# Performance work log

Hardware: AMD Instinct MI355X
Metric: run time of the kernel (lower is better)

Reference implementation:

```python
import jax, jax.numpy as jnp
import numpy as np

B, S, D, H = 8, 1024, 512, 8
DK = D // H
NEG = -1e30  # stands in for -inf; masked probs are zero-filled afterwards, so math matches


def setup_inputs() -> dict:
    rng = jax.random.key(0)
    ks = jax.random.split(rng, 12)
    f = lambda k, shape: jax.random.normal(k, shape, dtype=jnp.float32)
    w = lambda k: f(k, (D, D)) * 0.02  # stored as (in, out); y = x @ W + b
    return {
        "query": f(ks[0], (B, S, D)),
        "key": f(ks[1], (B, S, D)),
        "value": f(ks[2], (B, S, D)),
        "mask": jax.random.randint(ks[3], (B, 1, S), 0, 2, dtype=jnp.int32),
        "Wq": w(ks[4]), "bq": jnp.zeros((D,), jnp.float32),
        "Wk": w(ks[5]), "bk": jnp.zeros((D,), jnp.float32),
        "Wv": w(ks[6]), "bv": jnp.zeros((D,), jnp.float32),
        "Wo": w(ks[7]), "bo": jnp.zeros((D,), jnp.float32),
    }


def reference(query, key, value, mask, Wq, bq, Wk, bk, Wv, bv, Wo, bo):
    # QKV projections -> (B, H, S, DK)
    def proj(x, W, b):
        return (x @ W + b).reshape(B, -1, H, DK).transpose(0, 2, 1, 3)

    q = proj(query, Wq, bq)
    k = proj(key, Wk, bk)
    v = proj(value, Wv, bv)

    scores = jnp.einsum("bhqd,bhkd->bhqk", q, k) / jnp.sqrt(jnp.float32(DK))
    m = (mask[:, None, :, :] == 0)  # (B, 1, 1, S): True where masked out
    scores = jnp.where(m, NEG, scores)
    attn = jax.nn.softmax(scores, axis=-1)
    attn = jnp.where(m, 0.0, attn)  # dropout rate is 0.0 -> identity

    x = jnp.einsum("bhqk,bhkd->bhqd", attn, v)
    x = x.transpose(0, 2, 1, 3).reshape(B, -1, D)  # (B, S, D)
    return x @ Wo + bo
```

## Files before the change

kernel.cpp:

```cpp
#include <hip/hip_runtime.h>
#include <hip/hip_bf16.h>

#define NB 8
#define NS 1024
#define ND 512
#define NH 8
#define NDK 64

typedef __attribute__((ext_vector_type(8))) short bf16x8;
typedef __attribute__((ext_vector_type(4))) float f32x4;
typedef __attribute__((ext_vector_type(16))) float f32x16;

#define QSCALE 0.18033688011112042f
#define NEGBIG -3.0e38f

#define CVTPK(dst, a, b) \
    asm("v_cvt_pk_bf16_f32 %0, %1, %2" : "=v"(dst) : "v"(a), "v"(b))
#define PLSWAP(a, b) \
    asm("v_permlane32_swap_b32 %0, %1" : "+v"(a), "+v"(b))
#define GLOAD16(gp, lp)                                                        \
    __builtin_amdgcn_global_load_lds(                                          \
        (const __attribute__((address_space(1))) unsigned*)(gp),               \
        (__attribute__((address_space(3))) unsigned*)(lp), 16, 0, 0)
#define VMCNT0() asm volatile("s_waitcnt vmcnt(0)" ::: "memory")
#define SBAR() __builtin_amdgcn_s_barrier()
#define SCHED0() __builtin_amdgcn_sched_barrier(0)

__device__ __forceinline__ unsigned short bfround(float f) {
    union { float f; unsigned u; } v; v.f = f;
    unsigned u = v.u;
    u += 0x7fffu + ((u >> 16) & 1u);
    return (unsigned short)(u >> 16);
}

__device__ __forceinline__ size_t qf_off(int s, int dk) {
    return ((size_t)(((s >> 5) * 4 + (dk >> 4)) * 64 + ((dk >> 3) & 1) * 32 + (s & 31)) << 3) + (dk & 7);
}
__device__ __forceinline__ size_t kf_off(int s, int dk) {
    return ((size_t)(((s >> 6) * 8 + ((s >> 5) & 1) * 4 + (dk >> 4)) * 64 + ((dk >> 3) & 1) * 32 + (s & 31)) << 3) + (dk & 7);
}
__device__ __forceinline__ size_t vf_off(int s, int dk) {
    return ((size_t)(((s >> 6) * 8 + (dk >> 5) * 4 + ((s >> 4) & 3)) * 64 + ((s >> 3) & 1) * 32 + (dk & 31)) << 3) + (s & 7);
}

__global__ __launch_bounds__(256) void wt_kernel(const float* __restrict__ W0,
                                                 const float* __restrict__ W1,
                                                 const float* __restrict__ W2,
                                                 const float* __restrict__ W3,
                                                 unsigned short* __restrict__ wt) {
    __shared__ float sh[64][65];
    const int z = blockIdx.z;
    const float* W = z == 0 ? W0 : z == 1 ? W1 : z == 2 ? W2 : W3;
    unsigned short* out = wt + (size_t)z * ND * ND;
    const int o0 = blockIdx.x * 64, i0 = blockIdx.y * 64;
    const int tx = threadIdx.x & 63;
    const int ty = threadIdx.x >> 6;
    #pragma unroll
    for (int rr = 0; rr < 16; ++rr) {
        const int row = ty * 16 + rr;
        sh[row][tx] = W[(size_t)(i0 + row) * ND + o0 + tx];
    }
    __syncthreads();
    #pragma unroll
    for (int rr = 0; rr < 16; ++rr) {
        const int row = ty * 16 + rr;
        out[(size_t)(o0 + row) * ND + i0 + tx] = bfround(sh[tx][row]);
    }
}

__global__ __launch_bounds__(256) void gemm_qkv(
    const float* __restrict__ A0, const float* __restrict__ A1, const float* __restrict__ A2,
    const unsigned short* __restrict__ wt,
    const float* __restrict__ b0, const float* __restrict__ b1, const float* __restrict__ b2,
    unsigned short* __restrict__ outb) {
    __shared__ float Asf[2][128 * 32];
    __shared__ unsigned short Bs[2][128 * 32];
    const int t = threadIdx.x;
    const int lane = t & 63, w = t >> 6;
    const int wr = w >> 1, wc = w & 1;
    const int lr = lane & 15, lg = lane >> 4;
    const int bid = blockIdx.x;
    const int u = (bid & 7) * 96 + (bid >> 3);
    const int xt = u & 3, yt = (u >> 2) & 63, z = u >> 8;
    const float* A = z == 0 ? A0 : z == 1 ? A1 : A2;
    const float* bias = z == 0 ? b0 : z == 1 ? b1 : b2;
    const unsigned short* Wt = wt + (size_t)z * ND * ND;
    unsigned short* outp = outb + (size_t)z * NB * NH * NS * NDK;
    const int m0 = yt * 128, n0 = xt * 128;

    const int a_row = w * 32 + (lane >> 3);
    const int a_gc = ((lane & 7) ^ (lane >> 3)) << 2;
    const int b_row = w * 32 + (lane >> 2);
    const int b_gc = (lane & 3) * 8;

    f32x4 acc[4][4];
    #pragma unroll
    for (int i = 0; i < 4; ++i)
        #pragma unroll
        for (int j = 0; j < 4; ++j) acc[i][j] = (f32x4){0.f, 0.f, 0.f, 0.f};

#define QKV_STAGE(p, kt) do {                                                  \
        const int _k0 = (kt) * 32;                                             \
        GLOAD16(A + (size_t)(m0 + a_row + 0)  * ND + _k0 + a_gc, &Asf[p][(w * 4 + 0) * 256]); \
        GLOAD16(A + (size_t)(m0 + a_row + 8)  * ND + _k0 + a_gc, &Asf[p][(w * 4 + 1) * 256]); \
        GLOAD16(A + (size_t)(m0 + a_row + 16) * ND + _k0 + a_gc, &Asf[p][(w * 4 + 2) * 256]); \
        GLOAD16(A + (size_t)(m0 + a_row + 24) * ND + _k0 + a_gc, &Asf[p][(w * 4 + 3) * 256]); \
        GLOAD16(Wt + (size_t)(n0 + b_row + 0)  * ND + _k0 + b_gc, &Bs[p][(w * 2 + 0) * 512]); \
        GLOAD16(Wt + (size_t)(n0 + b_row + 16) * ND + _k0 + b_gc, &Bs[p][(w * 2 + 1) * 512]); \
    } while (0)

#define QKV_COMPUTE(p) do {                                                    \
        const float* _Ab = &Asf[p][0];                                         \
        const unsigned short* _Bb = &Bs[p][0];                                 \
        bf16x8 af[4], bfr[4];                                                  \
        _Pragma("unroll")                                                      \
        for (int mi = 0; mi < 4; ++mi) {                                       \
            const int r = wr * 64 + mi * 16 + lr;                              \
            const int u0 = (2 * lg) ^ (lr & 7);                                \
            const f32x4 x0 = *(const f32x4*)(_Ab + r * 32 + u0 * 4);           \
            const f32x4 x1 = *(const f32x4*)(_Ab + r * 32 + (u0 ^ 1) * 4);     \
            unsigned c0, c1, c2, c3;                                           \
            CVTPK(c0, x0[0], x0[1]); CVTPK(c1, x0[2], x0[3]);                  \
            CVTPK(c2, x1[0], x1[1]); CVTPK(c3, x1[2], x1[3]);                  \
            union { unsigned uu[4]; bf16x8 v; } cc;                            \
            cc.uu[0] = c0; cc.uu[1] = c1; cc.uu[2] = c2; cc.uu[3] = c3;        \
            af[mi] = cc.v;                                                     \
        }                                                                      \
        _Pragma("unroll")                                                      \
        for (int nj = 0; nj < 4; ++nj)                                         \
            bfr[nj] = *(const bf16x8*)(_Bb + (wc * 64 + nj * 16 + lr) * 32 + lg * 8); \
        __builtin_amdgcn_s_setprio(1);                                         \
        _Pragma("unroll")                                                      \
        for (int mi = 0; mi < 4; ++mi)                                         \
            _Pragma("unroll")                                                  \
            for (int nj = 0; nj < 4; ++nj)                                     \
                acc[mi][nj] = __builtin_amdgcn_mfma_f32_16x16x32_bf16(         \
                    af[mi], bfr[nj], acc[mi][nj], 0, 0, 0);                    \
        __builtin_amdgcn_s_setprio(0);                                         \
    } while (0)

    QKV_STAGE(0, 0);
    VMCNT0();
    SBAR();
    #pragma unroll 1
    for (int ii = 0; ii < 8; ++ii) {
        QKV_STAGE(1, 2 * ii + 1);
        SCHED0();
        QKV_COMPUTE(0);
        SCHED0();
        VMCNT0();
        SBAR();
        if (ii < 7) { QKV_STAGE(0, 2 * ii + 2); }
        SCHED0();
        QKV_COMPUTE(1);
        SCHED0();
        VMCNT0();
        SBAR();
    }
#undef QKV_STAGE
#undef QKV_COMPUTE

    const float osc = z == 0 ? QSCALE : 1.0f;
    #pragma unroll
    for (int mi = 0; mi < 4; ++mi) {
        #pragma unroll
        for (int nj = 0; nj < 4; ++nj) {
            const int n = n0 + wc * 64 + nj * 16 + lr;
            const float bv = bias[n];
            #pragma unroll
            for (int r = 0; r < 4; ++r) {
                const int m = m0 + wr * 64 + mi * 16 + lg * 4 + r;
                const float val = (acc[mi][nj][r] + bv) * osc;
                const int bb = m >> 10, s = m & 1023;
                const int hh = n >> 6, dk = n & 63;
                const size_t off = z == 0 ? qf_off(s, dk)
                                 : z == 1 ? kf_off(s, dk)
                                          : vf_off(s, dk);
                outp[((size_t)(bb * NH + hh) << 16) + off] = bfround(val);
            }
        }
    }
}

__global__ __launch_bounds__(256) void gemm_out(
    const unsigned short* __restrict__ Xb, const unsigned short* __restrict__ Wt,
    const float* __restrict__ bo, float* __restrict__ outp) {
    __shared__ unsigned short As2[2][128 * 32];
    __shared__ unsigned short Bs2[2][64 * 32];
    const int t = threadIdx.x;
    const int lane = t & 63, w = t >> 6;
    const int wr = w >> 1, wc = w & 1;
    const int lr = lane & 15, lg = lane >> 4;
    const int bid = blockIdx.x;
    const int u = (bid & 7) * 64 + (bid >> 3);
    const int xt = u & 7, yt = u >> 3;
    const int m0 = yt * 128, n0 = xt * 64;

    const int a_row = w * 32 + (lane >> 2);
    const int b_row = w * 16 + (lane >> 2);
    const int gc = (lane & 3) * 8;

    f32x4 acc[4][2];
    #pragma unroll
    for (int i = 0; i < 4; ++i)
        #pragma unroll
        for (int j = 0; j < 2; ++j) acc[i][j] = (f32x4){0.f, 0.f, 0.f, 0.f};

#define OUT_STAGE(p, kt) do {                                                  \
        const int _k0 = (kt) * 32;                                             \
        GLOAD16(Xb + (size_t)(m0 + a_row + 0)  * ND + _k0 + gc, &As2[p][(w * 2 + 0) * 512]); \
        GLOAD16(Xb + (size_t)(m0 + a_row + 16) * ND + _k0 + gc, &As2[p][(w * 2 + 1) * 512]); \
        GLOAD16(Wt + (size_t)(n0 + b_row) * ND + _k0 + gc, &Bs2[p][w * 512]);  \
    } while (0)

#define OUT_COMPUTE(p) do {                                                    \
        const unsigned short* _Ab = &As2[p][0];                                \
        const unsigned short* _Bb = &Bs2[p][0];                                \
        bf16x8 af[4], bfr[2];                                                  \
        _Pragma("unroll")                                                      \
        for (int mi = 0; mi < 4; ++mi)                                         \
            af[mi] = *(const bf16x8*)(_Ab + (wr * 64 + mi * 16 + lr) * 32 + lg * 8); \
        _Pragma("unroll")                                                      \
        for (int nj = 0; nj < 2; ++nj)                                         \
            bfr[nj] = *(const bf16x8*)(_Bb + (wc * 32 + nj * 16 + lr) * 32 + lg * 8); \
        __builtin_amdgcn_s_setprio(1);                                         \
        _Pragma("unroll")                                                      \
        for (int mi = 0; mi < 4; ++mi)                                         \
            _Pragma("unroll")                                                  \
            for (int nj = 0; nj < 2; ++nj)                                     \
                acc[mi][nj] = __builtin_amdgcn_mfma_f32_16x16x32_bf16(         \
                    af[mi], bfr[nj], acc[mi][nj], 0, 0, 0);                    \
        __builtin_amdgcn_s_setprio(0);                                         \
    } while (0)

    OUT_STAGE(0, 0);
    VMCNT0();
    SBAR();
    #pragma unroll 1
    for (int ii = 0; ii < 8; ++ii) {
        OUT_STAGE(1, 2 * ii + 1);
        SCHED0();
        OUT_COMPUTE(0);
        SCHED0();
        VMCNT0();
        SBAR();
        if (ii < 7) { OUT_STAGE(0, 2 * ii + 2); }
        SCHED0();
        OUT_COMPUTE(1);
        SCHED0();
        VMCNT0();
        SBAR();
    }
#undef OUT_STAGE
#undef OUT_COMPUTE

    #pragma unroll
    for (int mi = 0; mi < 4; ++mi) {
        #pragma unroll
        for (int nj = 0; nj < 2; ++nj) {
            const int n = n0 + wc * 32 + nj * 16 + lr;
            const float bv = bo[n];
            #pragma unroll
            for (int r = 0; r < 4; ++r) {
                const int m = m0 + wr * 64 + mi * 16 + lg * 4 + r;
                outp[(size_t)m * ND + n] = acc[mi][nj][r] + bv;
            }
        }
    }
}

struct AttnState {
    f32x16 acc0, acc1;
    float m_st, l_st;
};

__device__ __forceinline__ void attn_step(const bf16x8 (&kf)[8], const bf16x8 (&vv)[8],
                                          const bf16x8 (&qf)[4], int mval,
                                          float* __restrict__ brow, int lane, int hi,
                                          AttnState& st) {
    brow[lane] = mval ? 0.f : NEGBIG;

    f32x16 sc0 = {}, sc1 = {};
    __builtin_amdgcn_s_setprio(1);
    sc0 = __builtin_amdgcn_mfma_f32_32x32x16_bf16(kf[0], qf[0], sc0, 0, 0, 0);
    sc1 = __builtin_amdgcn_mfma_f32_32x32x16_bf16(kf[4], qf[0], sc1, 0, 0, 0);
    sc0 = __builtin_amdgcn_mfma_f32_32x32x16_bf16(kf[1], qf[1], sc0, 0, 0, 0);
    sc1 = __builtin_amdgcn_mfma_f32_32x32x16_bf16(kf[5], qf[1], sc1, 0, 0, 0);
    sc0 = __builtin_amdgcn_mfma_f32_32x32x16_bf16(kf[2], qf[2], sc0, 0, 0, 0);
    sc1 = __builtin_amdgcn_mfma_f32_32x32x16_bf16(kf[6], qf[2], sc1, 0, 0, 0);
    sc0 = __builtin_amdgcn_mfma_f32_32x32x16_bf16(kf[3], qf[3], sc0, 0, 0, 0);
    sc1 = __builtin_amdgcn_mfma_f32_32x32x16_bf16(kf[7], qf[3], sc1, 0, 0, 0);
    __builtin_amdgcn_s_setprio(0);

    {
        const float* bl = brow + 4 * hi;
        #pragma unroll
        for (int mm = 0; mm < 4; ++mm) {
            const f32x4 bv0 = *(const f32x4*)(bl + 8 * mm);
            const f32x4 bv1 = *(const f32x4*)(bl + 32 + 8 * mm);
            #pragma unroll
            for (int c = 0; c < 4; ++c) {
                sc0[4 * mm + c] += bv0[c];
                sc1[4 * mm + c] += bv1[c];
            }
        }
    }

    float tv[16];
    #pragma unroll
    for (int r = 0; r < 16; ++r) tv[r] = fmaxf(sc0[r], sc1[r]);
    #pragma unroll
    for (int s = 8; s > 0; s >>= 1)
        #pragma unroll
        for (int r = 0; r < 16; ++r)
            if (r < s) tv[r] = fmaxf(tv[r], tv[r + s]);
    const float mx = fmaxf(tv[0], __shfl_xor(tv[0], 32));
    const float mn = fmaxf(st.m_st, mx);

    #pragma unroll
    for (int r = 0; r < 16; ++r) {
        sc0[r] = __builtin_amdgcn_exp2f(sc0[r] - mn);
        sc1[r] = __builtin_amdgcn_exp2f(sc1[r] - mn);
    }
    #pragma unroll
    for (int r = 0; r < 16; ++r) tv[r] = sc0[r] + sc1[r];
    #pragma unroll
    for (int s = 8; s > 0; s >>= 1)
        #pragma unroll
        for (int r = 0; r < 16; ++r)
            if (r < s) tv[r] += tv[r + s];
    const float rs = tv[0] + __shfl_xor(tv[0], 32);

    const bool ch = mn > st.m_st;
    if (__any(ch)) {
        const float f = __builtin_amdgcn_exp2f(st.m_st - mn);
        st.l_st = st.l_st * f + rs;
        st.m_st = mn;
        #pragma unroll
        for (int r = 0; r < 16; ++r) { st.acc0[r] *= f; st.acc1[r] *= f; }
    } else {
        st.l_st += rs;
    }

    union U8 { unsigned u[4]; bf16x8 v; };
    bf16x8 pA0, pA1, pB0, pB1;
    {
        unsigned w00, w01, w10, w11, w20, w21, w30, w31;
        CVTPK(w00, sc0[0], sc0[1]);  CVTPK(w01, sc0[2], sc0[3]);
        CVTPK(w10, sc0[4], sc0[5]);  CVTPK(w11, sc0[6], sc0[7]);
        CVTPK(w20, sc0[8], sc0[9]);  CVTPK(w21, sc0[10], sc0[11]);
        CVTPK(w30, sc0[12], sc0[13]); CVTPK(w31, sc0[14], sc0[15]);
        PLSWAP(w00, w10); PLSWAP(w01, w11);
        PLSWAP(w20, w30); PLSWAP(w21, w31);
        U8 f0; f0.u[0] = w00; f0.u[1] = w01; f0.u[2] = w10; f0.u[3] = w11;
        U8 f1; f1.u[0] = w20; f1.u[1] = w21; f1.u[2] = w30; f1.u[3] = w31;
        pA0 = f0.v; pA1 = f1.v;
    }
    {
        unsigned w00, w01, w10, w11, w20, w21, w30, w31;
        CVTPK(w00, sc1[0], sc1[1]);  CVTPK(w01, sc1[2], sc1[3]);
        CVTPK(w10, sc1[4], sc1[5]);  CVTPK(w11, sc1[6], sc1[7]);
        CVTPK(w20, sc1[8], sc1[9]);  CVTPK(w21, sc1[10], sc1[11]);
        CVTPK(w30, sc1[12], sc1[13]); CVTPK(w31, sc1[14], sc1[15]);
        PLSWAP(w00, w10); PLSWAP(w01, w11);
        PLSWAP(w20, w30); PLSWAP(w21, w31);
        U8 f0; f0.u[0] = w00; f0.u[1] = w01; f0.u[2] = w10; f0.u[3] = w11;
        U8 f1; f1.u[0] = w20; f1.u[1] = w21; f1.u[2] = w30; f1.u[3] = w31;
        pB0 = f0.v; pB1 = f1.v;
    }

    __builtin_amdgcn_s_setprio(1);
    st.acc0 = __builtin_amdgcn_mfma_f32_32x32x16_bf16(vv[0], pA0, st.acc0, 0, 0, 0);
    st.acc1 = __builtin_amdgcn_mfma_f32_32x32x16_bf16(vv[4], pA0, st.acc1, 0, 0, 0);
    st.acc0 = __builtin_amdgcn_mfma_f32_32x32x16_bf16(vv[1], pA1, st.acc0, 0, 0, 0);
    st.acc1 = __builtin_amdgcn_mfma_f32_32x32x16_bf16(vv[5], pA1, st.acc1, 0, 0, 0);
    st.acc0 = __builtin_amdgcn_mfma_f32_32x32x16_bf16(vv[2], pB0, st.acc0, 0, 0, 0);
    st.acc1 = __builtin_amdgcn_mfma_f32_32x32x16_bf16(vv[6], pB0, st.acc1, 0, 0, 0);
    st.acc0 = __builtin_amdgcn_mfma_f32_32x32x16_bf16(vv[3], pB1, st.acc0, 0, 0, 0);
    st.acc1 = __builtin_amdgcn_mfma_f32_32x32x16_bf16(vv[7], pB1, st.acc1, 0, 0, 0);
    __builtin_amdgcn_s_setprio(0);
}

__global__ __launch_bounds__(256, 2) void attn_kernel(const unsigned short* __restrict__ QF,
                                                      const unsigned short* __restrict__ KF,
                                                      const unsigned short* __restrict__ VF,
                                                      const int* __restrict__ mask,
                                                      unsigned short* __restrict__ Xb) {
    __shared__ float bias_lds[4][64];
    const int t = threadIdx.x;
    const int lane = t & 63, w = t >> 6;
    const int q32 = lane & 31, hi = lane >> 5;
    const int bid = blockIdx.x;
    const int u = (bid & 7) * 64 + (bid >> 3);
    const int bh = u >> 3, xq = u & 7;
    const int b = bh >> 3, h = bh & 7;
    const int q = xq * 128 + w * 32 + q32;
    const unsigned short* QFh = QF + ((size_t)bh << 16);
    const unsigned short* KFh = KF + ((size_t)bh << 16);
    const unsigned short* VFh = VF + ((size_t)bh << 16);
    const int* mk = mask + b * NS;
    float* brow = &bias_lds[w][0];

    bf16x8 qf[4];
    {
        const unsigned short* Qp = QFh + (size_t)(xq * 16 + w * 4) * 512 + lane * 8;
        qf[0] = *(const bf16x8*)(Qp + 0 * 512);
        qf[1] = *(const bf16x8*)(Qp + 1 * 512);
        qf[2] = *(const bf16x8*)(Qp + 2 * 512);
        qf[3] = *(const bf16x8*)(Qp + 3 * 512);
    }

    AttnState st;
    st.acc0 = (f32x16){}; st.acc1 = (f32x16){};
    st.m_st = -1.0e30f; st.l_st = 0.f;

    bf16x8 kA[8], kB[8], vv[8];

#define LOADK(dst, itx) do {                                                   \
        const unsigned short* _p = KFh + (size_t)(itx) * 4096 + lane * 8;      \
        dst[0] = *(const bf16x8*)(_p + 0 * 512);                               \
        dst[1] = *(const bf16x8*)(_p + 1 * 512);                               \
        dst[2] = *(const bf16x8*)(_p + 2 * 512);                               \
        dst[3] = *(const bf16x8*)(_p + 3 * 512);                               \
        dst[4] = *(const bf16x8*)(_p + 4 * 512);                               \
        dst[5] = *(const bf16x8*)(_p + 5 * 512);                               \
        dst[6] = *(const bf16x8*)(_p + 6 * 512);                               \
        dst[7] = *(const bf16x8*)(_p + 7 * 512);                               \
    } while (0)

#define LOADV(dst, itx) do {                                                   \
        const unsigned short* _p = VFh + (size_t)(itx) * 4096 + lane * 8;      \
        dst[0] = *(const bf16x8*)(_p + 0 * 512);                               \
        dst[1] = *(const bf16x8*)(_p + 1 * 512);                               \
        dst[2] = *(const bf16x8*)(_p + 2 * 512);                               \
        dst[3] = *(const bf16x8*)(_p + 3 * 512);                               \
        dst[4] = *(const bf16x8*)(_p + 4 * 512);                               \
        dst[5] = *(const bf16x8*)(_p + 5 * 512);                               \
        dst[6] = *(const bf16x8*)(_p + 6 * 512);                               \
        dst[7] = *(const bf16x8*)(_p + 7 * 512);                               \
    } while (0)

    LOADK(kA, 0);
    #pragma unroll 1
    for (int ii = 0; ii < 8; ++ii) {
        const int itE = ii * 2, itO = itE + 1;
        const int mE = mk[itE * 64 + lane];
        LOADV(vv, itE);
        LOADK(kB, itO);
        __builtin_amdgcn_sched_barrier(0);
        attn_step(kA, vv, qf, mE, brow, lane, hi, st);
        const int mO = mk[itO * 64 + lane];
        const int itN = itO + 1 > 15 ? 15 : itO + 1;
        LOADV(vv, itO);
        LOADK(kA, itN);
        __builtin_amdgcn_sched_barrier(0);
        attn_step(kB, vv, qf, mO, brow, lane, hi, st);
    }
#undef LOADK
#undef LOADV

    const float inv = st.l_st > 0.f ? 1.f / st.l_st : 0.f;
    unsigned short* Xp = Xb + (size_t)(b * NS + q) * ND + h * 64 + 4 * hi;
    #pragma unroll
    for (int mm = 0; mm < 4; ++mm) {
        unsigned w0, w1;
        CVTPK(w0, st.acc0[4 * mm] * inv, st.acc0[4 * mm + 1] * inv);
        CVTPK(w1, st.acc0[4 * mm + 2] * inv, st.acc0[4 * mm + 3] * inv);
        uint2 pv; pv.x = w0; pv.y = w1;
        *(uint2*)(Xp + 8 * mm) = pv;
        CVTPK(w0, st.acc1[4 * mm] * inv, st.acc1[4 * mm + 1] * inv);
        CVTPK(w1, st.acc1[4 * mm + 2] * inv, st.acc1[4 * mm + 3] * inv);
        pv.x = w0; pv.y = w1;
        *(uint2*)(Xp + 32 + 8 * mm) = pv;
    }
}

extern "C" void kernel_launch(void* const* d_in, const int* in_sizes, int n_in,
                              void* d_out, int out_size, void* d_ws, size_t ws_size,
                              hipStream_t stream) {
    const float* query = (const float*)d_in[0];
    const float* key   = (const float*)d_in[1];
    const float* value = (const float*)d_in[2];
    const int*   mask  = (const int*)d_in[3];
    const float* Wq = (const float*)d_in[4];
    const float* bq = (const float*)d_in[5];
    const float* Wk = (const float*)d_in[6];
    const float* bk = (const float*)d_in[7];
    const float* Wv = (const float*)d_in[8];
    const float* bv = (const float*)d_in[9];
    const float* Wo = (const float*)d_in[10];
    const float* bo = (const float*)d_in[11];

    const size_t HEADSZ = (size_t)NB * NH * NS * NDK;
    unsigned short* wt = (unsigned short*)d_ws;
    unsigned short* QFb = wt + (size_t)4 * ND * ND;
    unsigned short* KFb = QFb + HEADSZ;
    unsigned short* VFb = KFb + HEADSZ;
    unsigned short* Xb  = VFb + HEADSZ;

    wt_kernel<<<dim3(8, 8, 4), 256, 0, stream>>>(Wq, Wk, Wv, Wo, wt);

    gemm_qkv<<<768, 256, 0, stream>>>(query, key, value, wt, bq, bk, bv, QFb);

    attn_kernel<<<512, 256, 0, stream>>>(QFb, KFb, VFb, mask, Xb);

    gemm_out<<<512, 256, 0, stream>>>(Xb, wt + (size_t)3 * ND * ND, bo, (float*)d_out);
}
```

Before: 82.83 us.

## Replace direct global-to-LDS loads with register-staged padded LDS pipeline in GEMMs

Both projection GEMMs stop using global_load_lds and instead load tiles into registers, then write them to padded LDS buffers (row stride 40). In the QKV GEMM the fp32-to-bf16 conversion moves from the LDS read side to the register write side, so LDS holds bf16 instead of fp32. The loop becomes a register-prefetch double buffer with one barrier per k-step. This trades more VGPRs and extra LDS write instructions for less LDS traffic and smaller conversion work per compute step, at some risk to the overlap the previous async-copy scheme provided.

```diff
diff --git a/kernel.cpp b/kernel.cpp
--- a/kernel.cpp
+++ b/kernel.cpp
@@ -18,13 +18,6 @@
     asm("v_cvt_pk_bf16_f32 %0, %1, %2" : "=v"(dst) : "v"(a), "v"(b))
 #define PLSWAP(a, b) \
     asm("v_permlane32_swap_b32 %0, %1" : "+v"(a), "+v"(b))
-#define GLOAD16(gp, lp)                                                        \
-    __builtin_amdgcn_global_load_lds(                                          \
-        (const __attribute__((address_space(1))) unsigned*)(gp),               \
-        (__attribute__((address_space(3))) unsigned*)(lp), 16, 0, 0)
-#define VMCNT0() asm volatile("s_waitcnt vmcnt(0)" ::: "memory")
-#define SBAR() __builtin_amdgcn_s_barrier()
-#define SCHED0() __builtin_amdgcn_sched_barrier(0)
 
 __device__ __forceinline__ unsigned short bfround(float f) {
     union { float f; unsigned u; } v; v.f = f;
@@ -73,8 +66,8 @@
     const unsigned short* __restrict__ wt,
     const float* __restrict__ b0, const float* __restrict__ b1, const float* __restrict__ b2,
     unsigned short* __restrict__ outb) {
-    __shared__ float Asf[2][128 * 32];
-    __shared__ unsigned short Bs[2][128 * 32];
+    __shared__ unsigned short Als[2][128 * 40];
+    __shared__ unsigned short Bls[2][128 * 40];
     const int t = threadIdx.x;
     const int lane = t & 63, w = t >> 6;
     const int wr = w >> 1, wc = w & 1;
@@ -89,9 +82,9 @@
     const int m0 = yt * 128, n0 = xt * 128;
 
     const int a_row = w * 32 + (lane >> 3);
-    const int a_gc = ((lane & 7) ^ (lane >> 3)) << 2;
+    const int a_col = (lane & 7) * 4;
     const int b_row = w * 32 + (lane >> 2);
-    const int b_gc = (lane & 3) * 8;
+    const int b_col = (lane & 3) * 8;
 
     f32x4 acc[4][4];
     #pragma unroll
@@ -99,36 +92,44 @@
         #pragma unroll
         for (int j = 0; j < 4; ++j) acc[i][j] = (f32x4){0.f, 0.f, 0.f, 0.f};
 
-#define QKV_STAGE(p, kt) do {                                                  \
+    f32x4 ra[4];
+    bf16x8 rbv[2];
+
+#define QKV_LOAD(kt) do {                                                      \
         const int _k0 = (kt) * 32;                                             \
-        GLOAD16(A + (size_t)(m0 + a_row + 0)  * ND + _k0 + a_gc, &Asf[p][(w * 4 + 0) * 256]); \
-        GLOAD16(A + (size_t)(m0 + a_row + 8)  * ND + _k0 + a_gc, &Asf[p][(w * 4 + 1) * 256]); \
-        GLOAD16(A + (size_t)(m0 + a_row + 16) * ND + _k0 + a_gc, &Asf[p][(w * 4 + 2) * 256]); \
-        GLOAD16(A + (size_t)(m0 + a_row + 24) * ND + _k0 + a_gc, &Asf[p][(w * 4 + 3) * 256]); \
-        GLOAD16(Wt + (size_t)(n0 + b_row + 0)  * ND + _k0 + b_gc, &Bs[p][(w * 2 + 0) * 512]); \
-        GLOAD16(Wt + (size_t)(n0 + b_row + 16) * ND + _k0 + b_gc, &Bs[p][(w * 2 + 1) * 512]); \
+        ra[0] = *(const f32x4*)(A + (size_t)(m0 + a_row + 0)  * ND + _k0 + a_col); \
+        ra[1] = *(const f32x4*)(A + (size_t)(m0 + a_row + 8)  * ND + _k0 + a_col); \
+        ra[2] = *(const f32x4*)(A + (size_t)(m0 + a_row + 16) * ND + _k0 + a_col); \
+        ra[3] = *(const f32x4*)(A + (size_t)(m0 + a_row + 24) * ND + _k0 + a_col); \
+        rbv[0] = *(const bf16x8*)(Wt + (size_t)(n0 + b_row + 0)  * ND + _k0 + b_col); \
+        rbv[1] = *(const bf16x8*)(Wt + (size_t)(n0 + b_row + 16) * ND + _k0 + b_col); \
+    } while (0)
+
+#define QKV_WRITE(p) do {                                                      \
+        _Pragma("unroll")                                                      \
+        for (int j = 0; j < 4; ++j) {                                          \
+            unsigned c0, c1;                                                   \
+            CVTPK(c0, ra[j][0], ra[j][1]);                                     \
+            CVTPK(c1, ra[j][2], ra[j][3]);                                     \
+            uint2 pv; pv.x = c0; pv.y = c1;                                    \
+            *(uint2*)(&Als[p][(a_row + j * 8) * 40 + a_col]) = pv;             \
+        }                                                                      \
+        _Pragma("unroll")                                                      \
+        for (int j = 0; j < 2; ++j) {                                          \
+            union { bf16x8 v; uint2 h[2]; } ub; ub.v = rbv[j];                 \
+            *(uint2*)(&Bls[p][(b_row + j * 16) * 40 + b_col]) = ub.h[0];       \
+            *(uint2*)(&Bls[p][(b_row + j * 16) * 40 + b_col + 4]) = ub.h[1];   \
+        }                                                                      \
     } while (0)
 
 #define QKV_COMPUTE(p) do {                                                    \
-        const float* _Ab = &Asf[p][0];                                         \
-        const unsigned short* _Bb = &Bs[p][0];                                 \
         bf16x8 af[4], bfr[4];                                                  \
         _Pragma("unroll")                                                      \
-        for (int mi = 0; mi < 4; ++mi) {                                       \
-            const int r = wr * 64 + mi * 16 + lr;                              \
-            const int u0 = (2 * lg) ^ (lr & 7);                                \
-            const f32x4 x0 = *(const f32x4*)(_Ab + r * 32 + u0 * 4);           \
-            const f32x4 x1 = *(const f32x4*)(_Ab + r * 32 + (u0 ^ 1) * 4);     \
-            unsigned c0, c1, c2, c3;                                           \
-            CVTPK(c0, x0[0], x0[1]); CVTPK(c1, x0[2], x0[3]);                  \
-            CVTPK(c2, x1[0], x1[1]); CVTPK(c3, x1[2], x1[3]);                  \
-            union { unsigned uu[4]; bf16x8 v; } cc;                            \
-            cc.uu[0] = c0; cc.uu[1] = c1; cc.uu[2] = c2; cc.uu[3] = c3;        \
-            af[mi] = cc.v;                                                     \
-        }                                                                      \
+        for (int mi = 0; mi < 4; ++mi)                                         \
+            af[mi] = *(const bf16x8*)(&Als[p][(wr * 64 + mi * 16 + lr) * 40 + lg * 8]); \
         _Pragma("unroll")                                                      \
         for (int nj = 0; nj < 4; ++nj)                                         \
-            bfr[nj] = *(const bf16x8*)(_Bb + (wc * 64 + nj * 16 + lr) * 32 + lg * 8); \
+            bfr[nj] = *(const bf16x8*)(&Bls[p][(wc * 64 + nj * 16 + lr) * 40 + lg * 8]); \
         __builtin_amdgcn_s_setprio(1);                                         \
         _Pragma("unroll")                                                      \
         for (int mi = 0; mi < 4; ++mi)                                         \
@@ -139,25 +140,20 @@
         __builtin_amdgcn_s_setprio(0);                                         \
     } while (0)
 
-    QKV_STAGE(0, 0);
-    VMCNT0();
-    SBAR();
+    QKV_LOAD(0);
+    QKV_WRITE(0);
+    QKV_LOAD(1);
+    __syncthreads();
     #pragma unroll 1
-    for (int ii = 0; ii < 8; ++ii) {
-        QKV_STAGE(1, 2 * ii + 1);
-        SCHED0();
-        QKV_COMPUTE(0);
-        SCHED0();
-        VMCNT0();
-        SBAR();
-        if (ii < 7) { QKV_STAGE(0, 2 * ii + 2); }
-        SCHED0();
-        QKV_COMPUTE(1);
-        SCHED0();
-        VMCNT0();
-        SBAR();
-    }
-#undef QKV_STAGE
+    for (int kt = 0; kt < 15; ++kt) {
+        QKV_COMPUTE(kt & 1);
+        QKV_WRITE((kt + 1) & 1);
+        if (kt < 14) QKV_LOAD(kt + 2);
+        __syncthreads();
+    }
+    QKV_COMPUTE(1);
+#undef QKV_LOAD
+#undef QKV_WRITE
 #undef QKV_COMPUTE
 
     const float osc = z == 0 ? QSCALE : 1.0f;
@@ -185,8 +181,8 @@
 __global__ __launch_bounds__(256) void gemm_out(
     const unsigned short* __restrict__ Xb, const unsigned short* __restrict__ Wt,
     const float* __restrict__ bo, float* __restrict__ outp) {
-    __shared__ unsigned short As2[2][128 * 32];
-    __shared__ unsigned short Bs2[2][64 * 32];
+    __shared__ unsigned short Ao[2][128 * 40];
+    __shared__ unsigned short Bo[2][64 * 40];
     const int t = threadIdx.x;
     const int lane = t & 63, w = t >> 6;
     const int wr = w >> 1, wc = w & 1;
@@ -206,23 +202,37 @@
         #pragma unroll
         for (int j = 0; j < 2; ++j) acc[i][j] = (f32x4){0.f, 0.f, 0.f, 0.f};
 
-#define OUT_STAGE(p, kt) do {                                                  \
+    bf16x8 raa[2], rbb;
+
+#define OUT_LOAD(kt) do {                                                      \
         const int _k0 = (kt) * 32;                                             \
-        GLOAD16(Xb + (size_t)(m0 + a_row + 0)  * ND + _k0 + gc, &As2[p][(w * 2 + 0) * 512]); \
-        GLOAD16(Xb + (size_t)(m0 + a_row + 16) * ND + _k0 + gc, &As2[p][(w * 2 + 1) * 512]); \
-        GLOAD16(Wt + (size_t)(n0 + b_row) * ND + _k0 + gc, &Bs2[p][w * 512]);  \
+        raa[0] = *(const bf16x8*)(Xb + (size_t)(m0 + a_row + 0)  * ND + _k0 + gc); \
+        raa[1] = *(const bf16x8*)(Xb + (size_t)(m0 + a_row + 16) * ND + _k0 + gc); \
+        rbb    = *(const bf16x8*)(Wt + (size_t)(n0 + b_row) * ND + _k0 + gc);  \
+    } while (0)
+
+#define OUT_WRITE(p) do {                                                      \
+        _Pragma("unroll")                                                      \
+        for (int j = 0; j < 2; ++j) {                                          \
+            union { bf16x8 v; uint2 h[2]; } ua; ua.v = raa[j];                 \
+            *(uint2*)(&Ao[p][(a_row + j * 16) * 40 + gc]) = ua.h[0];           \
+            *(uint2*)(&Ao[p][(a_row + j * 16) * 40 + gc + 4]) = ua.h[1];       \
+        }                                                                      \
+        {                                                                      \
+            union { bf16x8 v; uint2 h[2]; } ub; ub.v = rbb;                    \
+            *(uint2*)(&Bo[p][b_row * 40 + gc]) = ub.h[0];                      \
+            *(uint2*)(&Bo[p][b_row * 40 + gc + 4]) = ub.h[1];                  \
+        }                                                                      \
     } while (0)
 
 #define OUT_COMPUTE(p) do {                                                    \
-        const unsigned short* _Ab = &As2[p][0];                                \
-        const unsigned short* _Bb = &Bs2[p][0];                                \
         bf16x8 af[4], bfr[2];                                                  \
         _Pragma("unroll")                                                      \
         for (int mi = 0; mi < 4; ++mi)                                         \
-            af[mi] = *(const bf16x8*)(_Ab + (wr * 64 + mi * 16 + lr) * 32 + lg * 8); \
+            af[mi] = *(const bf16x8*)(&Ao[p][(wr * 64 + mi * 16 + lr) * 40 + lg * 8]); \
         _Pragma("unroll")                                                      \
         for (int nj = 0; nj < 2; ++nj)                                         \
-            bfr[nj] = *(const bf16x8*)(_Bb + (wc * 32 + nj * 16 + lr) * 32 + lg * 8); \
+            bfr[nj] = *(const bf16x8*)(&Bo[p][(wc * 32 + nj * 16 + lr) * 40 + lg * 8]); \
         __builtin_amdgcn_s_setprio(1);                                         \
         _Pragma("unroll")                                                      \
         for (int mi = 0; mi < 4; ++mi)                                         \
@@ -233,25 +243,20 @@
         __builtin_amdgcn_s_setprio(0);                                         \
     } while (0)
 
-    OUT_STAGE(0, 0);
-    VMCNT0();
-    SBAR();
+    OUT_LOAD(0);
+    OUT_WRITE(0);
+    OUT_LOAD(1);
+    __syncthreads();
     #pragma unroll 1
-    for (int ii = 0; ii < 8; ++ii) {
-        OUT_STAGE(1, 2 * ii + 1);
-        SCHED0();
-        OUT_COMPUTE(0);
-        SCHED0();
-        VMCNT0();
-        SBAR();
-        if (ii < 7) { OUT_STAGE(0, 2 * ii + 2); }
-        SCHED0();
-        OUT_COMPUTE(1);
-        SCHED0();
-        VMCNT0();
-        SBAR();
-    }
-#undef OUT_STAGE
+    for (int kt = 0; kt < 15; ++kt) {
+        OUT_COMPUTE(kt & 1);
+        OUT_WRITE((kt + 1) & 1);
+        if (kt < 14) OUT_LOAD(kt + 2);
+        __syncthreads();
+    }
+    OUT_COMPUTE(1);
+#undef OUT_LOAD
+#undef OUT_WRITE
 #undef OUT_COMPUTE
 
     #pragma unroll
```

Result: no change. 81.99 us (-1.0%).
